# Kernel optimization log

Hardware: AMD Instinct MI355X
Metric: run time of the kernel (lower is better)

## Reference

```python
import jax, jax.numpy as jnp
import numpy as np
from jax import lax

NTIME = 2048
NCOMP = 8
HID = 64
OUT = 64
MAX_EVENTS = NTIME * NCOMP
EVENT_DIM = NCOMP + 3


def setup_inputs() -> dict:
    key = jax.random.key(0)
    ks = jax.random.split(key, 10)
    B = 64
    s = lambda fan_in: 1.0 / np.sqrt(fan_in)
    return {
        "x": jax.random.uniform(ks[0], (B, NTIME, NCOMP), dtype=jnp.float32),
        "W1": jax.random.normal(ks[1], (EVENT_DIM, HID), dtype=jnp.float32) * s(EVENT_DIM),
        "b1": jax.random.normal(ks[2], (HID,), dtype=jnp.float32) * 0.01,
        "W2": jax.random.normal(ks[3], (HID, HID), dtype=jnp.float32) * s(HID),
        "b2": jax.random.normal(ks[4], (HID,), dtype=jnp.float32) * 0.01,
        "P1": jax.random.normal(ks[5], (HID + 1, HID), dtype=jnp.float32) * s(HID + 1),
        "pb1": jax.random.normal(ks[6], (HID,), dtype=jnp.float32) * 0.01,
        "P2": jax.random.normal(ks[7], (HID, OUT), dtype=jnp.float32) * s(HID),
        "pb2": jax.random.normal(ks[8], (OUT,), dtype=jnp.float32) * 0.01,
    }


def _event_table(x):
    # x: [B, T, C] float. Vectorized run-length encoding.
    B, T, C = x.shape
    seq = jnp.transpose((x > 0.5).astype(x.dtype), (0, 2, 1))  # [B, C, T] in {0,1}
    prev = jnp.concatenate([jnp.full((B, C, 1), -1.0, x.dtype), seq[:, :, :-1]], axis=-1)
    is_start = seq != prev  # t=0 always a start; [B, C, T] bool
    t_idx = jnp.arange(T, dtype=jnp.int32)
    # position of next run start strictly after t (T if none)
    start_pos = jnp.where(is_start, t_idx, T)  # [B, C, T] int32
    shifted = jnp.concatenate([start_pos[:, :, 1:], jnp.full((B, C, 1), T, jnp.int32)], axis=-1)
    next_start = lax.cummin(shifted, axis=2, reverse=True)  # suffix min
    dur = (next_start - t_idx).astype(x.dtype)  # run length at each start slot
    max_start = max(1, T - 1)
    start_norm = (t_idx.astype(x.dtype) / max_start)  # [T]
    onehot = jnp.broadcast_to(jnp.eye(C, dtype=x.dtype)[None, :, None, :], (B, C, T, C))
    feats = jnp.stack(
        [seq, jnp.broadcast_to(start_norm, (B, C, T)), dur / T], axis=-1
    )  # [B, C, T, 3]
    rows = jnp.concatenate([onehot, feats], axis=-1)  # [B, C, T, C+3]
    mask = is_start
    rows = rows * mask[..., None].astype(x.dtype)  # masked rows zero, as in torch
    return rows.reshape(B, C * T, C + 3), mask.reshape(B, C * T)


def reference(x, W1, b1, W2, b2, P1, pb1, P2, pb2):
    rows, mask = _event_table(x)  # [B, E, 11], [B, E]
    h = jax.nn.relu(rows @ W1 + b1) @ W2 + b2  # [B, E, HID]
    h = h * mask[..., None].astype(h.dtype)
    valid = jnp.maximum(mask.sum(axis=1, keepdims=True), 1).astype(h.dtype)  # [B, 1]
    pooled = h.sum(axis=1) / valid  # [B, HID]
    z = jnp.concatenate([pooled, valid / MAX_EVENTS], axis=-1)  # [B, HID+1]
    return jax.nn.relu(z @ P1 + pb1) @ P2 + pb2  # [B, OUT]
```

## Files before the change

### kernel.cpp

```cpp
#include <hip/hip_runtime.h>
#include <hip/hip_bf16.h>
#include <hip/hip_fp16.h>

#define T_LEN 2048
#define NCOMP 8
#define HID 64
#define OUT_DIM 64
#define BATCH 64
#define MAX_EVENTS (T_LEN * NCOMP)
#define NCHUNK 32
#define PART_STRIDE 66
#define NWAVE 8

typedef unsigned long long u64;

#define PARTIAL_BYTES (64ULL * NCOMP * PART_STRIDE * 4)

static __device__ inline unsigned pack_f16pair(int a, int b) {
    __half ha = __float2half_rn((float)a);
    __half hb = __float2half_rn((float)b);
    return (unsigned)__half_as_ushort(ha) | ((unsigned)__half_as_ushort(hb) << 16);
}

__global__ __launch_bounds__(512) void event_kernel(
    const float* __restrict__ x,
    const float* __restrict__ W1,
    const float* __restrict__ b1,
    float* __restrict__ partial)
{
    const int b    = blockIdx.x & 63;
    const int c    = blockIdx.x >> 6;
    const int tid  = threadIdx.x;
    const int lane = tid & 63;
    const int wave = tid >> 6;

    __shared__ u64 wsh[NCHUNK];
    __shared__ u64 tsh[NCHUNK];
    __shared__ int nxtf[NCHUNK + 1];
    __shared__ int wtot[NWAVE];
    __shared__ unsigned elist[T_LEN];
    __shared__ float Sp[NWAVE][HID];

    const float4* xp = (const float4*)(x + ((size_t)b * T_LEN) * NCOMP);
    #pragma unroll
    for (int i = 0; i < 4; ++i) {
        int t = i * 512 + tid;
        float4 v0 = xp[t * 2];
        float4 v1 = xp[t * 2 + 1];
        unsigned m = 0;
        m |= (v0.x > 0.5f) ? 1u   : 0u;
        m |= (v0.y > 0.5f) ? 2u   : 0u;
        m |= (v0.z > 0.5f) ? 4u   : 0u;
        m |= (v0.w > 0.5f) ? 8u   : 0u;
        m |= (v1.x > 0.5f) ? 16u  : 0u;
        m |= (v1.y > 0.5f) ? 32u  : 0u;
        m |= (v1.z > 0.5f) ? 64u  : 0u;
        m |= (v1.w > 0.5f) ? 128u : 0u;
        u64 wd = __ballot((m >> c) & 1u);
        if (lane == 0) wsh[i * 8 + wave] = wd;
    }
    __syncthreads();

    if (tid < NCHUNK) {
        u64 w = wsh[tid];
        u64 carry = (tid > 0) ? (wsh[tid - 1] >> 63) : 0ULL;
        u64 tr = w ^ ((w << 1) | carry);
        if (tid == 0) tr |= 1ULL;
        tsh[tid] = tr;
        int first = tr ? tid * 64 + (__ffsll((long long)tr) - 1) : T_LEN;
        #pragma unroll
        for (int off = 1; off < NCHUNK; off <<= 1) {
            int v = __shfl_down(first, off);
            if (tid + off < NCHUNK) first = (v < first) ? v : first;
        }
        nxtf[tid] = first;
        if (tid == 0) nxtf[NCHUNK] = T_LEN;
    }
    __syncthreads();

    const int s0 = (int)(wsh[0] & 1ULL);

    const int ch = tid >> 4;
    const int sh = (tid & 15) * 4;
    const u64 full = tsh[ch];
    unsigned tr4 = (unsigned)((full >> sh) & 0xFu);
    int nt = __popc(tr4);

    int incl = nt;
    #pragma unroll
    for (int o = 1; o < 64; o <<= 1) {
        int v = __shfl_up(incl, o);
        if (lane >= o) incl += v;
    }
    if (lane == 63) wtot[wave] = incl;
    __syncthreads();
    int waveoff = 0;
    for (int w = 0; w < wave; ++w) waveoff += wtot[w];
    int nE = 0;
    #pragma unroll
    for (int w = 0; w < NWAVE; ++w) nE += wtot[w];
    int off = waveoff + incl - nt;

    unsigned rem = tr4;
    while (rem) {
        int p = __ffs(rem) - 1;
        rem &= rem - 1;
        int t = (tid << 2) + p;
        int nxt;
        if (rem) {
            nxt = (tid << 2) + __ffs(rem) - 1;
        } else {
            int bp = sh + 4;
            u64 above = (bp >= 64) ? 0ULL : (full & (~0ULL << bp));
            nxt = above ? ch * 64 + (__ffsll((long long)above) - 1) : nxtf[ch + 1];
        }
        elist[off++] = pack_f16pair(t, nxt);
    }
    __syncthreads();

    const float r8    = W1[8 * HID + lane];
    const float r9p   = W1[9 * HID + lane] * (1.0f / 2047.0f);
    const float r10p  = W1[10 * HID + lane] * (1.0f / 2048.0f);
    const float r9m   = r9p - r10p;
    const float base0 = W1[c * HID + lane] + b1[lane];
    const float base1 = base0 + r8;
    const float baseEven = s0 ? base1 : base0;
    const float baseOdd  = s0 ? base0 : base1;

    const int span = ((nE + 31) >> 5) << 2;
    const int i0   = wave * span;
    const int i1   = (i0 + span < nE) ? (i0 + span) : nE;

    float S0 = 0.0f, S1 = 0.0f, S2 = 0.0f, S3 = 0.0f;
    int i = i0;
    for (; i + 3 < i1; i += 4) {
        uint4 e = *(const uint4*)&elist[i];
        __half2 h0 = *reinterpret_cast<__half2*>(&e.x);
        __half2 h1 = *reinterpret_cast<__half2*>(&e.y);
        __half2 h2 = *reinterpret_cast<__half2*>(&e.z);
        __half2 h3 = *reinterpret_cast<__half2*>(&e.w);
        float a0 = fmaf(__high2float(h0), r10p, baseEven);
        float a1 = fmaf(__high2float(h1), r10p, baseOdd);
        float a2 = fmaf(__high2float(h2), r10p, baseEven);
        float a3 = fmaf(__high2float(h3), r10p, baseOdd);
        a0 = fmaf(__low2float(h0), r9m, a0);
        a1 = fmaf(__low2float(h1), r9m, a1);
        a2 = fmaf(__low2float(h2), r9m, a2);
        a3 = fmaf(__low2float(h3), r9m, a3);
        S0 += fmaxf(a0, 0.0f);
        S1 += fmaxf(a1, 0.0f);
        S2 += fmaxf(a2, 0.0f);
        S3 += fmaxf(a3, 0.0f);
    }
    for (; i < i1; ++i) {
        unsigned eu = elist[i];
        __half2 h = *reinterpret_cast<__half2*>(&eu);
        float base = (i & 1) ? baseOdd : baseEven;
        float a = fmaf(__high2float(h), r10p, base);
        a = fmaf(__low2float(h), r9m, a);
        S0 += fmaxf(a, 0.0f);
    }
    Sp[wave][lane] = (S0 + S1) + (S2 + S3);
    __syncthreads();

    float* pp = partial + ((size_t)b * NCOMP + c) * PART_STRIDE;
    if (tid < HID) {
        float s = 0.0f;
        #pragma unroll
        for (int w = 0; w < NWAVE; ++w) s += Sp[w][tid];
        pp[tid] = s;
    }
    if (tid == HID) pp[HID] = (float)nE;
}

__global__ __launch_bounds__(64) void head_kernel(
    const float* __restrict__ partial,
    const float* __restrict__ W2,
    const float* __restrict__ b2,
    const float* __restrict__ P1,
    const float* __restrict__ pb1,
    const float* __restrict__ P2,
    const float* __restrict__ pb2,
    float* __restrict__ out)
{
    const int b = blockIdx.x;
    const int h = threadIdx.x;

    __shared__ float sb[HID];
    __shared__ float z[HID + 1];
    __shared__ float y[HID];

    float s = 0.0f, cnt = 0.0f;
    #pragma unroll
    for (int cc = 0; cc < NCOMP; ++cc) {
        const float* pp = partial + ((size_t)b * NCOMP + cc) * PART_STRIDE;
        s   += pp[h];
        cnt += pp[HID];
    }
    float valid = fmaxf(cnt, 1.0f);
    sb[h] = s;
    __syncthreads();

    float acc = 0.0f;
    #pragma unroll
    for (int k = 0; k < HID; ++k) acc = fmaf(sb[k], W2[k * HID + h], acc);
    z[h] = acc / valid + b2[h];
    if (h == 0) z[HID] = valid / (float)MAX_EVENTS;
    __syncthreads();

    float a1 = pb1[h];
    #pragma unroll
    for (int k = 0; k < HID + 1; ++k) a1 = fmaf(z[k], P1[k * HID + h], a1);
    y[h] = fmaxf(a1, 0.0f);
    __syncthreads();

    float o = pb2[h];
    #pragma unroll
    for (int k = 0; k < HID; ++k) o = fmaf(y[k], P2[k * HID + h], o);
    out[(size_t)b * OUT_DIM + h] = o;
}

extern "C" void kernel_launch(void* const* d_in, const int* in_sizes, int n_in,
                              void* d_out, int out_size, void* d_ws, size_t ws_size,
                              hipStream_t stream) {
    const float* x   = (const float*)d_in[0];
    const float* W1  = (const float*)d_in[1];
    const float* b1  = (const float*)d_in[2];
    const float* W2  = (const float*)d_in[3];
    const float* b2  = (const float*)d_in[4];
    const float* P1  = (const float*)d_in[5];
    const float* pb1 = (const float*)d_in[6];
    const float* P2  = (const float*)d_in[7];
    const float* pb2 = (const float*)d_in[8];
    float* out = (float*)d_out;

    float* partial = (float*)d_ws;

    event_kernel<<<BATCH * NCOMP, 512, 0, stream>>>(x, W1, b1, partial);
    head_kernel<<<BATCH, 64, 0, stream>>>(partial, W2, b2, P1, pb1, P2, pb2, out);
}
```

Before: 17.08 us.

## Split event accumulation across hidden-dim groups and parallelize head kernel K-loop

In the event kernel, each lane now handles 4 hidden dims for one of 4 interleaved event groups, instead of one hidden dim across all of its wave's events. Partial sums are then combined with cross-lane shuffles. Each wave walks its event span with 4 lanes in parallel rather than serially, which shortens the per-lane dependent loop. The head kernel goes from 64 to 256 threads, splitting each matmul's K dimension into 4 quarters reduced through shared memory, at the cost of extra barriers.

After: 16.24 us. 1.05x faster.

```diff
diff --git a/kernel.cpp b/kernel.cpp
--- a/kernel.cpp
+++ b/kernel.cpp
@@ -118,49 +118,83 @@
     }
     __syncthreads();
 
-    const float r8    = W1[8 * HID + lane];
-    const float r9p   = W1[9 * HID + lane] * (1.0f / 2047.0f);
-    const float r10p  = W1[10 * HID + lane] * (1.0f / 2048.0f);
-    const float r9m   = r9p - r10p;
-    const float base0 = W1[c * HID + lane] + b1[lane];
-    const float base1 = base0 + r8;
-    const float baseEven = s0 ? base1 : base0;
-    const float baseOdd  = s0 ? base0 : base1;
-
-    const int span = ((nE + 31) >> 5) << 2;
+    const int dg = lane & 15;
+    const int eg = lane >> 4;
+
+    const float4 w9  = *(const float4*)&W1[9 * HID + 4 * dg];
+    const float4 w10 = *(const float4*)&W1[10 * HID + 4 * dg];
+    const float4 w8  = *(const float4*)&W1[8 * HID + 4 * dg];
+    const float4 wc  = *(const float4*)&W1[c * HID + 4 * dg];
+    const float4 bb  = *(const float4*)&b1[4 * dg];
+
+    const float r10p0 = w10.x * (1.0f / 2048.0f);
+    const float r10p1 = w10.y * (1.0f / 2048.0f);
+    const float r10p2 = w10.z * (1.0f / 2048.0f);
+    const float r10p3 = w10.w * (1.0f / 2048.0f);
+    const float r9m0  = w9.x * (1.0f / 2047.0f) - r10p0;
+    const float r9m1  = w9.y * (1.0f / 2047.0f) - r10p1;
+    const float r9m2  = w9.z * (1.0f / 2047.0f) - r10p2;
+    const float r9m3  = w9.w * (1.0f / 2047.0f) - r10p3;
+    const float b00 = wc.x + bb.x, b01 = wc.y + bb.y;
+    const float b02 = wc.z + bb.z, b03 = wc.w + bb.w;
+    const float b10 = b00 + w8.x, b11 = b01 + w8.y;
+    const float b12 = b02 + w8.z, b13 = b03 + w8.w;
+    const float beE0 = s0 ? b10 : b00, beO0 = s0 ? b00 : b10;
+    const float beE1 = s0 ? b11 : b01, beO1 = s0 ? b01 : b11;
+    const float beE2 = s0 ? b12 : b02, beO2 = s0 ? b02 : b12;
+    const float beE3 = s0 ? b13 : b03, beO3 = s0 ? b03 : b13;
+
+    const int span = ((nE + NWAVE * 16 - 1) >> 7) << 4;
     const int i0   = wave * span;
     const int i1   = (i0 + span < nE) ? (i0 + span) : nE;
 
     float S0 = 0.0f, S1 = 0.0f, S2 = 0.0f, S3 = 0.0f;
-    int i = i0;
-    for (; i + 3 < i1; i += 4) {
+
+#define EV_ACC(tf, nf, BE)                                            \
+    S0 += fmaxf(fmaf(tf, r9m0, fmaf(nf, r10p0, BE##0)), 0.0f);        \
+    S1 += fmaxf(fmaf(tf, r9m1, fmaf(nf, r10p1, BE##1)), 0.0f);        \
+    S2 += fmaxf(fmaf(tf, r9m2, fmaf(nf, r10p2, BE##2)), 0.0f);        \
+    S3 += fmaxf(fmaf(tf, r9m3, fmaf(nf, r10p3, BE##3)), 0.0f);
+
+    int i = i0 + 4 * eg;
+    for (; i + 3 < i1; i += 16) {
         uint4 e = *(const uint4*)&elist[i];
-        __half2 h0 = *reinterpret_cast<__half2*>(&e.x);
-        __half2 h1 = *reinterpret_cast<__half2*>(&e.y);
-        __half2 h2 = *reinterpret_cast<__half2*>(&e.z);
-        __half2 h3 = *reinterpret_cast<__half2*>(&e.w);
-        float a0 = fmaf(__high2float(h0), r10p, baseEven);
-        float a1 = fmaf(__high2float(h1), r10p, baseOdd);
-        float a2 = fmaf(__high2float(h2), r10p, baseEven);
-        float a3 = fmaf(__high2float(h3), r10p, baseOdd);
-        a0 = fmaf(__low2float(h0), r9m, a0);
-        a1 = fmaf(__low2float(h1), r9m, a1);
-        a2 = fmaf(__low2float(h2), r9m, a2);
-        a3 = fmaf(__low2float(h3), r9m, a3);
-        S0 += fmaxf(a0, 0.0f);
-        S1 += fmaxf(a1, 0.0f);
-        S2 += fmaxf(a2, 0.0f);
-        S3 += fmaxf(a3, 0.0f);
-    }
-    for (; i < i1; ++i) {
-        unsigned eu = elist[i];
-        __half2 h = *reinterpret_cast<__half2*>(&eu);
-        float base = (i & 1) ? baseOdd : baseEven;
-        float a = fmaf(__high2float(h), r10p, base);
-        a = fmaf(__low2float(h), r9m, a);
-        S0 += fmaxf(a, 0.0f);
-    }
-    Sp[wave][lane] = (S0 + S1) + (S2 + S3);
+        __half2 h0 = *reinterpret_cast<const __half2*>(&e.x);
+        __half2 h1 = *reinterpret_cast<const __half2*>(&e.y);
+        __half2 h2 = *reinterpret_cast<const __half2*>(&e.z);
+        __half2 h3 = *reinterpret_cast<const __half2*>(&e.w);
+        float t0 = __low2float(h0), n0 = __high2float(h0);
+        float t1 = __low2float(h1), n1 = __high2float(h1);
+        float t2 = __low2float(h2), n2 = __high2float(h2);
+        float t3 = __low2float(h3), n3 = __high2float(h3);
+        EV_ACC(t0, n0, beE)
+        EV_ACC(t1, n1, beO)
+        EV_ACC(t2, n2, beE)
+        EV_ACC(t3, n3, beO)
+    }
+    if (i < i1) {
+        for (int ii = i; ii < i1 && ii < i + 4; ++ii) {
+            unsigned eu = elist[ii];
+            __half2 hh = *reinterpret_cast<const __half2*>(&eu);
+            float tf = __low2float(hh), nf = __high2float(hh);
+            const int odd = ii & 1;
+            float B0 = odd ? beO0 : beE0, B1 = odd ? beO1 : beE1;
+            float B2 = odd ? beO2 : beE2, B3 = odd ? beO3 : beE3;
+            S0 += fmaxf(fmaf(tf, r9m0, fmaf(nf, r10p0, B0)), 0.0f);
+            S1 += fmaxf(fmaf(tf, r9m1, fmaf(nf, r10p1, B1)), 0.0f);
+            S2 += fmaxf(fmaf(tf, r9m2, fmaf(nf, r10p2, B2)), 0.0f);
+            S3 += fmaxf(fmaf(tf, r9m3, fmaf(nf, r10p3, B3)), 0.0f);
+        }
+    }
+#undef EV_ACC
+
+    S0 += __shfl_xor(S0, 16); S0 += __shfl_xor(S0, 32);
+    S1 += __shfl_xor(S1, 16); S1 += __shfl_xor(S1, 32);
+    S2 += __shfl_xor(S2, 16); S2 += __shfl_xor(S2, 32);
+    S3 += __shfl_xor(S3, 16); S3 += __shfl_xor(S3, 32);
+    if (eg == 0) {
+        *(float4*)&Sp[wave][4 * dg] = make_float4(S0, S1, S2, S3);
+    }
     __syncthreads();
 
     float* pp = partial + ((size_t)b * NCOMP + c) * PART_STRIDE;
@@ -173,7 +207,7 @@
     if (tid == HID) pp[HID] = (float)nE;
 }
 
-__global__ __launch_bounds__(64) void head_kernel(
+__global__ __launch_bounds__(256) void head_kernel(
     const float* __restrict__ partial,
     const float* __restrict__ W2,
     const float* __restrict__ b2,
@@ -183,41 +217,53 @@
     const float* __restrict__ pb2,
     float* __restrict__ out)
 {
-    const int b = blockIdx.x;
-    const int h = threadIdx.x;
-
+    const int b   = blockIdx.x;
+    const int tid = threadIdx.x;
+    const int h   = tid & 63;
+    const int q   = tid >> 6;
+
+    __shared__ float red[4][HID];
     __shared__ float sb[HID];
+    __shared__ float cnt8[8];
     __shared__ float z[HID + 1];
     __shared__ float y[HID];
 
-    float s = 0.0f, cnt = 0.0f;
-    #pragma unroll
-    for (int cc = 0; cc < NCOMP; ++cc) {
-        const float* pp = partial + ((size_t)b * NCOMP + cc) * PART_STRIDE;
-        s   += pp[h];
-        cnt += pp[HID];
-    }
-    float valid = fmaxf(cnt, 1.0f);
-    sb[h] = s;
-    __syncthreads();
+    const float* pb_ = partial + (size_t)b * NCOMP * PART_STRIDE;
+
+    red[q][h] = pb_[(2 * q) * PART_STRIDE + h] + pb_[(2 * q + 1) * PART_STRIDE + h];
+    if (tid < NCOMP) cnt8[tid] = pb_[tid * PART_STRIDE + HID];
+    __syncthreads();
+    if (q == 0) sb[h] = red[0][h] + red[1][h] + red[2][h] + red[3][h];
+    __syncthreads();
+    const float valid = fmaxf(cnt8[0] + cnt8[1] + cnt8[2] + cnt8[3] +
+                              cnt8[4] + cnt8[5] + cnt8[6] + cnt8[7], 1.0f);
 
     float acc = 0.0f;
     #pragma unroll
-    for (int k = 0; k < HID; ++k) acc = fmaf(sb[k], W2[k * HID + h], acc);
-    z[h] = acc / valid + b2[h];
-    if (h == 0) z[HID] = valid / (float)MAX_EVENTS;
-    __syncthreads();
-
-    float a1 = pb1[h];
-    #pragma unroll
-    for (int k = 0; k < HID + 1; ++k) a1 = fmaf(z[k], P1[k * HID + h], a1);
-    y[h] = fmaxf(a1, 0.0f);
-    __syncthreads();
-
-    float o = pb2[h];
-    #pragma unroll
-    for (int k = 0; k < HID; ++k) o = fmaf(y[k], P2[k * HID + h], o);
-    out[(size_t)b * OUT_DIM + h] = o;
+    for (int k = 16 * q; k < 16 * q + 16; ++k)
+        acc = fmaf(sb[k], W2[k * HID + h], acc);
+    red[q][h] = acc;
+    __syncthreads();
+    if (q == 0) z[h] = (red[0][h] + red[1][h] + red[2][h] + red[3][h]) / valid + b2[h];
+    if (tid == 0) z[HID] = valid / (float)MAX_EVENTS;
+    __syncthreads();
+
+    float a = (q == 0) ? fmaf(z[HID], P1[HID * HID + h], pb1[h]) : 0.0f;
+    #pragma unroll
+    for (int k = 16 * q; k < 16 * q + 16; ++k)
+        a = fmaf(z[k], P1[k * HID + h], a);
+    red[q][h] = a;
+    __syncthreads();
+    if (q == 0) y[h] = fmaxf(red[0][h] + red[1][h] + red[2][h] + red[3][h], 0.0f);
+    __syncthreads();
+
+    float o = (q == 0) ? pb2[h] : 0.0f;
+    #pragma unroll
+    for (int k = 16 * q; k < 16 * q + 16; ++k)
+        o = fmaf(y[k], P2[k * HID + h], o);
+    red[q][h] = o;
+    __syncthreads();
+    if (q == 0) out[(size_t)b * OUT_DIM + h] = red[0][h] + red[1][h] + red[2][h] + red[3][h];
 }
 
 extern "C" void kernel_launch(void* const* d_in, const int* in_sizes, int n_in,
@@ -237,5 +283,5 @@
     float* partial = (float*)d_ws;
 
     event_kernel<<<BATCH * NCOMP, 512, 0, stream>>>(x, W1, b1, partial);
-    head_kernel<<<BATCH, 64, 0, stream>>>(partial, W2, b2, P1, pb1, P2, pb2, out);
-}
+    head_kernel<<<BATCH, 256, 0, stream>>>(partial, W2, b2, P1, pb1, P2, pb2, out);
+}
```
